# Performance work log

Hardware: AMD Instinct MI355X
Metric: run time of the kernel (lower is better)

## Reference

```python
import jax, jax.numpy as jnp
import numpy as np

H = 16        # heads
DH = 64       # dim_head
DM = 1024     # query_dim = context_dim
INNER = H * DH


def setup_inputs() -> dict:
    key = jax.random.key(0)
    ks = jax.random.split(key, 5)
    s = 0.02
    queries = jax.random.normal(ks[0], (2, 2048, DM), dtype=jnp.float32)
    Wq = jax.random.normal(ks[1], (DM, INNER), dtype=jnp.float32) * s
    Wkv = jax.random.normal(ks[2], (DM, 2 * INNER), dtype=jnp.float32) * s
    Wo = jax.random.normal(ks[3], (INNER, DM), dtype=jnp.float32) * s
    bo = jax.random.normal(ks[4], (DM,), dtype=jnp.float32) * s
    return {"queries": queries, "Wq": Wq, "Wkv": Wkv, "Wo": Wo, "bo": bo}


def reference(queries, Wq, Wkv, Wo, bo):
    b, n, _ = queries.shape
    scale = DH ** -0.5
    q = queries @ Wq                       # [b, n, inner]
    kv = queries @ Wkv                     # self-attention: context = queries
    k, v = jnp.split(kv, 2, axis=-1)
    # b n (h d) -> b h n d
    split_heads = lambda t: t.reshape(b, n, H, DH).transpose(0, 2, 1, 3)
    q, k, v = map(split_heads, (q, k, v))
    sim = jnp.einsum('bhid,bhjd->bhij', q, k) * scale
    attn = jax.nn.softmax(sim, axis=-1)    # dropout is identity (p=0 / eval)
    out = jnp.einsum('bhij,bhjd->bhid', attn, v)
    out = out.transpose(0, 2, 1, 3).reshape(b, n, INNER)
    return out @ Wo + bo
```

## Files before the change

kernel.cpp:

```cpp
#include <hip/hip_runtime.h>
#include <math.h>
#include <stdint.h>

typedef _Float16 half8v __attribute__((ext_vector_type(8)));
typedef _Float16 half4v __attribute__((ext_vector_type(4)));
typedef _Float16 half2v __attribute__((ext_vector_type(2)));
typedef __fp16 fp16x2 __attribute__((ext_vector_type(2)));
typedef float floatx4 __attribute__((ext_vector_type(4)));

#define MFMA16(a, b, c) __builtin_amdgcn_mfma_f32_16x16x32_f16(a, b, c, 0, 0, 0)

#define QSCALE 0.18033688011112f

__device__ __forceinline__ void gld_lds16(const void* g, void* l) {
  __builtin_amdgcn_global_load_lds(
      (const __attribute__((address_space(1))) uint32_t*)(uintptr_t)g,
      (__attribute__((address_space(3))) uint32_t*)(uintptr_t)l, 16, 0, 0);
}

__device__ __forceinline__ half2v pk16(float a, float b) {
  fp16x2 t = __builtin_amdgcn_cvt_pkrtz(a, b);
  return __builtin_bit_cast(half2v, t);
}

__global__ __launch_bounds__(256) void convert_x(
    const float* __restrict__ X, _Float16* __restrict__ X16)
{
  size_t gid = (size_t)blockIdx.x * 256 + threadIdx.x;
  const float4* src = (const float4*)(X) + gid * 2;
  float4 a = src[0], b = src[1];
  half8v h;
  h[0]=(_Float16)a.x; h[1]=(_Float16)a.y; h[2]=(_Float16)a.z; h[3]=(_Float16)a.w;
  h[4]=(_Float16)b.x; h[5]=(_Float16)b.y; h[6]=(_Float16)b.z; h[7]=(_Float16)b.w;
  *((half8v*)X16 + gid) = h;
}

__global__ __launch_bounds__(256) void transpose_w(
    const float* __restrict__ Wq, const float* __restrict__ Wkv,
    const float* __restrict__ Wo,
    _Float16* __restrict__ WqkvT, _Float16* __restrict__ WoT)
{
  __shared__ alignas(16) _Float16 Tt[64 * 68];

  int b = blockIdx.x;
  const float* src; _Float16* dst; int N, tk, tn;
  if (b < 256)      { src = Wq;  dst = WqkvT;                 N = 1024; tk = b & 15;        tn = b >> 4; }
  else if (b < 768) { src = Wkv; dst = WqkvT + (size_t)1024 * 1024; N = 2048; tk = (b - 256) & 15; tn = (b - 256) >> 4; }
  else              { src = Wo;  dst = WoT;                   N = 1024; tk = (b - 768) & 15; tn = (b - 768) >> 4; }

  const int t = threadIdx.x;
  {
    int kg = t >> 4, ng = t & 15;
    const float* sp = src + (size_t)(tk * 64 + kg * 4) * N + tn * 64 + ng * 4;
    float4 r0 = *(const float4*)(sp);
    float4 r1 = *(const float4*)(sp + N);
    float4 r2 = *(const float4*)(sp + 2 * N);
    float4 r3 = *(const float4*)(sp + 3 * N);
    half4v h;
    h[0]=(_Float16)r0.x; h[1]=(_Float16)r1.x; h[2]=(_Float16)r2.x; h[3]=(_Float16)r3.x;
    *(half4v*)&Tt[(ng * 4 + 0) * 68 + kg * 4] = h;
    h[0]=(_Float16)r0.y; h[1]=(_Float16)r1.y; h[2]=(_Float16)r2.y; h[3]=(_Float16)r3.y;
    *(half4v*)&Tt[(ng * 4 + 1) * 68 + kg * 4] = h;
    h[0]=(_Float16)r0.z; h[1]=(_Float16)r1.z; h[2]=(_Float16)r2.z; h[3]=(_Float16)r3.z;
    *(half4v*)&Tt[(ng * 4 + 2) * 68 + kg * 4] = h;
    h[0]=(_Float16)r0.w; h[1]=(_Float16)r1.w; h[2]=(_Float16)r2.w; h[3]=(_Float16)r3.w;
    *(half4v*)&Tt[(ng * 4 + 3) * 68 + kg * 4] = h;
  }
  __syncthreads();
  #pragma unroll
  for (int i = 0; i < 2; i++) {
    int idx = t + i * 256;
    int nl = idx >> 3, k8 = (idx & 7) * 8;
    half8v v = *(half8v*)&Tt[nl * 68 + k8];
    *(half8v*)(dst + (size_t)(tn * 64 + nl) * 1024 + tk * 64 + k8) = v;
  }
}

__global__ __launch_bounds__(256) void qkv_gemm(
    const _Float16* __restrict__ X16, const _Float16* __restrict__ WqkvT,
    _Float16* __restrict__ q_ws, _Float16* __restrict__ k_ws,
    _Float16* __restrict__ vT_ws)
{
  constexpr int K = 1024;
  __shared__ alignas(16) _Float16 As[128 * 32];
  __shared__ alignas(16) _Float16 Bs[128 * 32];

  const int m0 = blockIdx.x * 128;
  const int n0 = blockIdx.y * 128;

  const int tid  = threadIdx.x;
  const int wave = tid >> 6, lane = tid & 63;
  const int qd = lane >> 4, l15 = lane & 15;
  const int wr = (wave >> 1) * 64, wc = (wave & 1) * 64;
  const int r0i = tid >> 2, c0 = (tid & 3) * 8;

  floatx4 acc[4][4] = {};

  for (int k0 = 0; k0 < K; k0 += 32) {
    gld_lds16(X16 + (size_t)(m0 + r0i) * K + k0 + c0, &As[tid * 8]);
    gld_lds16(X16 + (size_t)(m0 + 64 + r0i) * K + k0 + c0, &As[(tid + 256) * 8]);
    gld_lds16(WqkvT + (size_t)(n0 + r0i) * K + k0 + c0, &Bs[tid * 8]);
    gld_lds16(WqkvT + (size_t)(n0 + 64 + r0i) * K + k0 + c0, &Bs[(tid + 256) * 8]);
    __syncthreads();
    half8v a[4], b[4];
    #pragma unroll
    for (int it = 0; it < 4; it++)
      a[it] = *(half8v*)&As[(wr + it * 16 + l15) * 32 + qd * 8];
    #pragma unroll
    for (int jt = 0; jt < 4; jt++)
      b[jt] = *(half8v*)&Bs[(wc + jt * 16 + l15) * 32 + qd * 8];
    #pragma unroll
    for (int it = 0; it < 4; it++)
      #pragma unroll
      for (int jt = 0; jt < 4; jt++)
        acc[it][jt] = MFMA16(a[it], b[jt], acc[it][jt]);
    __syncthreads();
  }

  #pragma unroll
  for (int it = 0; it < 4; it++) {
    #pragma unroll
    for (int jt = 0; jt < 4; jt++) {
      #pragma unroll
      for (int r = 0; r < 4; r++) {
        int m = m0 + wr + it * 16 + qd * 4 + r;
        int n = n0 + wc + jt * 16 + l15;
        float val = acc[it][jt][r];
        int bb = m >> 11, nn = m & 2047;
        if (n0 < 1024) {
          int h = n >> 6, d = n & 63;
          q_ws[(((size_t)bb * 16 + h) * 2048 + nn) * 64 + d] = (_Float16)(val * QSCALE);
        } else if (n0 < 2048) {
          int c = n - 1024, h = c >> 6, d = c & 63;
          k_ws[(((size_t)bb * 16 + h) * 2048 + nn) * 64 + d] = (_Float16)val;
        } else {
          int c = n - 2048, h = c >> 6, d = c & 63;
          vT_ws[(((size_t)bb * 16 + h) * 64 + d) * 2048 + nn] = (_Float16)val;
        }
      }
    }
  }
}

__device__ __forceinline__ int swz(int row, int blk) {
  return row * 64 + ((blk ^ (row & 7)) << 3);
}

__global__ __launch_bounds__(128, 2) void attn_kernel(
    const _Float16* __restrict__ q_ws, const _Float16* __restrict__ k_ws,
    const _Float16* __restrict__ vT_ws, _Float16* __restrict__ aout)
{
  constexpr int N = 2048;
  __shared__ alignas(16) _Float16 Qs[64 * 64];
  __shared__ alignas(16) _Float16 Ks[2][64 * 64];
  __shared__ alignas(16) _Float16 Vts[2][64 * 64];

  const int id = blockIdx.x;
  const int bh = ((id >> 8) << 3) | (id & 7);
  const int qt = (id >> 3) & 31;

  const _Float16* Qp = q_ws + (size_t)bh * N * 64;
  const _Float16* Kp = k_ws + (size_t)bh * N * 64;
  const _Float16* Vp = vT_ws + (size_t)bh * 64 * N;

  const int tid = threadIdx.x, wave = tid >> 6, lane = tid & 63;
  const int qd = lane >> 4, l15 = lane & 15;
  const int q0 = qt * 64;
  const int wbase = wave * 32;

  #pragma unroll
  for (int i = 0; i < 4; i++) {
    int idx = tid + i * 128;
    int r = idx >> 3, blk = idx & 7;
    *(half8v*)&Qs[swz(r, blk)] =
        *(const half8v*)(Qp + (size_t)(q0 + r) * 64 + blk * 8);
  }
  __syncthreads();
  half8v qf[2][2];
  #pragma unroll
  for (int m = 0; m < 2; m++)
    #pragma unroll
    for (int ks = 0; ks < 2; ks++)
      qf[m][ks] = *(half8v*)&Qs[swz(wbase + m * 16 + l15, ks * 4 + qd)];

  floatx4 o[2][4] = {};
  float lsum[2] = {};

  half8v kpre[4], vpre[4];
  #pragma unroll
  for (int i = 0; i < 4; i++) {
    int idx = tid + i * 128;
    int r = idx >> 3, c8 = (idx & 7) * 8;
    kpre[i] = *(const half8v*)(Kp + (size_t)r * 64 + c8);
    vpre[i] = *(const half8v*)(Vp + (size_t)r * N + c8);
  }
  #pragma unroll
  for (int i = 0; i < 4; i++) {
    int idx = tid + i * 128;
    int r = idx >> 3, blk = idx & 7;
    *(half8v*)&Ks[0][swz(r, blk)]  = kpre[i];
    *(half8v*)&Vts[0][swz(r, blk)] = vpre[i];
  }

  int p = 0;
  for (int kv0 = 0; kv0 < N; kv0 += 64) {
    const bool more = (kv0 + 64) < N;
    if (more) {
      int kvn = kv0 + 64;
      #pragma unroll
      for (int i = 0; i < 4; i++) {
        int idx = tid + i * 128;
        int r = idx >> 3, c8 = (idx & 7) * 8;
        kpre[i] = *(const half8v*)(Kp + (size_t)(kvn + r) * 64 + c8);
        vpre[i] = *(const half8v*)(Vp + (size_t)r * N + kvn + c8);
      }
    }
    __syncthreads();

    floatx4 s[4][2] = {};
    #pragma unroll
    for (int ks = 0; ks < 2; ks++) {
      half8v kf[4];
      #pragma unroll
      for (int nt = 0; nt < 4; nt++)
        kf[nt] = *(half8v*)&Ks[p][swz(nt * 16 + l15, ks * 4 + qd)];
      #pragma unroll
      for (int nt = 0; nt < 4; nt++)
        #pragma unroll
        for (int m = 0; m < 2; m++)
          s[nt][m] = MFMA16(kf[nt], qf[m][ks], s[nt][m]);
    }

    #pragma unroll
    for (int m = 0; m < 2; m++) {
      #pragma unroll
      for (int nt = 0; nt < 4; nt++) {
        float p0 = __builtin_amdgcn_exp2f(s[nt][m][0]);
        float p1 = __builtin_amdgcn_exp2f(s[nt][m][1]);
        float p2 = __builtin_amdgcn_exp2f(s[nt][m][2]);
        float p3 = __builtin_amdgcn_exp2f(s[nt][m][3]);
        lsum[m] += (p0 + p1) + (p2 + p3);
        half2v h01 = pk16(p0, p1);
        half2v h23 = pk16(p2, p3);
        half4v pk;
        pk[0] = h01[0]; pk[1] = h01[1]; pk[2] = h23[0]; pk[3] = h23[1];
        *(half4v*)&Qs[swz(wbase + m * 16 + l15, 2 * nt + (qd >> 1)) +
                      (qd & 1) * 4] = pk;
      }
    }

    #pragma unroll
    for (int ks = 0; ks < 2; ks++) {
      half8v pf[2], vf[4];
      #pragma unroll
      for (int m = 0; m < 2; m++)
        pf[m] = *(half8v*)&Qs[swz(wbase + m * 16 + l15, 4 * ks + qd)];
      #pragma unroll
      for (int nt = 0; nt < 4; nt++)
        vf[nt] = *(half8v*)&Vts[p][swz(nt * 16 + l15, 4 * ks + qd)];
      #pragma unroll
      for (int m = 0; m < 2; m++)
        #pragma unroll
        for (int nt = 0; nt < 4; nt++)
          o[m][nt] = MFMA16(pf[m], vf[nt], o[m][nt]);
    }

    if (more) {
      #pragma unroll
      for (int i = 0; i < 4; i++) {
        int idx = tid + i * 128;
        int r = idx >> 3, blk = idx & 7;
        *(half8v*)&Ks[p ^ 1][swz(r, blk)]  = kpre[i];
        *(half8v*)&Vts[p ^ 1][swz(r, blk)] = vpre[i];
      }
    }
    p ^= 1;
  }

  #pragma unroll
  for (int m = 0; m < 2; m++) {
    lsum[m] += __shfl_xor(lsum[m], 16);
    lsum[m] += __shfl_xor(lsum[m], 32);
  }

  const int bb = bh >> 4, hh = bh & 15;
  #pragma unroll
  for (int m = 0; m < 2; m++) {
    #pragma unroll
    for (int r = 0; r < 4; r++) {
      float inv = 1.0f / __shfl(lsum[m], qd * 4 + r);
      int n = q0 + wbase + m * 16 + qd * 4 + r;
      #pragma unroll
      for (int dt = 0; dt < 4; dt++) {
        int d = dt * 16 + l15;
        aout[((size_t)(bb * 2048 + n)) * 1024 + hh * 64 + d] =
            (_Float16)(o[m][dt][r] * inv);
      }
    }
  }
}

__global__ __launch_bounds__(256) void out_gemm(
    const _Float16* __restrict__ A, const _Float16* __restrict__ WoT,
    const float* __restrict__ bo, float* __restrict__ Out)
{
  constexpr int K = 1024;
  __shared__ alignas(16) _Float16 As[128 * 32];
  __shared__ alignas(16) _Float16 Bs[128 * 32];

  const int m0 = blockIdx.x * 128;
  const int n0 = blockIdx.y * 128;
  const int tid = threadIdx.x;
  const int wave = tid >> 6, lane = tid & 63;
  const int qd = lane >> 4, l15 = lane & 15;
  const int wr = (wave >> 1) * 64, wc = (wave & 1) * 64;
  const int r0i = tid >> 2, c0 = (tid & 3) * 8;

  floatx4 acc[4][4] = {};

  for (int k0 = 0; k0 < K; k0 += 32) {
    gld_lds16(A + (size_t)(m0 + r0i) * K + k0 + c0, &As[tid * 8]);
    gld_lds16(A + (size_t)(m0 + 64 + r0i) * K + k0 + c0, &As[(tid + 256) * 8]);
    gld_lds16(WoT + (size_t)(n0 + r0i) * K + k0 + c0, &Bs[tid * 8]);
    gld_lds16(WoT + (size_t)(n0 + 64 + r0i) * K + k0 + c0, &Bs[(tid + 256) * 8]);
    __syncthreads();
    half8v a[4], b[4];
    #pragma unroll
    for (int it = 0; it < 4; it++)
      a[it] = *(half8v*)&As[(wr + it * 16 + l15) * 32 + qd * 8];
    #pragma unroll
    for (int jt = 0; jt < 4; jt++)
      b[jt] = *(half8v*)&Bs[(wc + jt * 16 + l15) * 32 + qd * 8];
    #pragma unroll
    for (int it = 0; it < 4; it++)
      #pragma unroll
      for (int jt = 0; jt < 4; jt++)
        acc[it][jt] = MFMA16(a[it], b[jt], acc[it][jt]);
    __syncthreads();
  }

  #pragma unroll
  for (int it = 0; it < 4; it++) {
    #pragma unroll
    for (int jt = 0; jt < 4; jt++) {
      int n = n0 + wc + jt * 16 + l15;
      float bias = bo[n];
      #pragma unroll
      for (int r = 0; r < 4; r++) {
        int m = m0 + wr + it * 16 + qd * 4 + r;
        Out[(size_t)m * 1024 + n] = acc[it][jt][r] + bias;
      }
    }
  }
}

extern "C" void kernel_launch(void* const* d_in, const int* in_sizes, int n_in,
                              void* d_out, int out_size, void* d_ws, size_t ws_size,
                              hipStream_t stream) {
  const float* X   = (const float*)d_in[0];
  const float* Wq  = (const float*)d_in[1];
  const float* Wkv = (const float*)d_in[2];
  const float* Wo  = (const float*)d_in[3];
  const float* bo  = (const float*)d_in[4];
  float* out = (float*)d_out;

  const size_t M4 = (size_t)4 * 1024 * 1024;
  _Float16* q_ws   = (_Float16*)d_ws;
  _Float16* k_ws   = q_ws + M4;
  _Float16* vT_ws  = k_ws + M4;
  _Float16* X16    = vT_ws + M4;
  _Float16* WqkvT  = X16 + M4;
  _Float16* WoT    = WqkvT + (size_t)3 * 1024 * 1024;
  _Float16* aout   = X16;

  convert_x<<<2048, 256, 0, stream>>>(X, X16);
  transpose_w<<<1024, 256, 0, stream>>>(Wq, Wkv, Wo, WqkvT, WoT);
  qkv_gemm<<<dim3(32, 24), 256, 0, stream>>>(X16, WqkvT, q_ws, k_ws, vT_ws);
  attn_kernel<<<1024, 128, 0, stream>>>(q_ws, k_ws, vT_ws, aout);
  out_gemm<<<dim3(32, 8), 256, 0, stream>>>(aout, WoT, bo, out);
}
```

Measured before the change: 197.8 us.

## Enlarge attention query tile to 128 rows per block and restructure QK loop

Each attention block now processes 128 query rows instead of 64, with each wave owning 64 rows, which halves the grid and halves the K/V tile traffic per query row. The QK^T computation is reorganised to loop over key subtiles, computing and exponentiating one 16-column strip at a time, which limits live score registers. The trade-off is higher accumulator register pressure (16 output tiles per wave), which may lower occupancy, and only 512 blocks to spread across the CUs.

```diff
diff --git a/kernel.cpp b/kernel.cpp
--- a/kernel.cpp
+++ b/kernel.cpp
@@ -151,13 +151,13 @@
     const _Float16* __restrict__ vT_ws, _Float16* __restrict__ aout)
 {
   constexpr int N = 2048;
-  __shared__ alignas(16) _Float16 Qs[64 * 64];
+  __shared__ alignas(16) _Float16 Qs[128 * 64];
   __shared__ alignas(16) _Float16 Ks[2][64 * 64];
   __shared__ alignas(16) _Float16 Vts[2][64 * 64];
 
   const int id = blockIdx.x;
-  const int bh = ((id >> 8) << 3) | (id & 7);
-  const int qt = (id >> 3) & 31;
+  const int bh = ((id >> 7) << 3) | (id & 7);
+  const int qt = (id >> 3) & 15;
 
   const _Float16* Qp = q_ws + (size_t)bh * N * 64;
   const _Float16* Kp = k_ws + (size_t)bh * N * 64;
@@ -165,26 +165,26 @@
 
   const int tid = threadIdx.x, wave = tid >> 6, lane = tid & 63;
   const int qd = lane >> 4, l15 = lane & 15;
-  const int q0 = qt * 64;
-  const int wbase = wave * 32;
-
-  #pragma unroll
-  for (int i = 0; i < 4; i++) {
+  const int q0 = qt * 128;
+  const int wbase = wave * 64;
+
+  #pragma unroll
+  for (int i = 0; i < 8; i++) {
     int idx = tid + i * 128;
     int r = idx >> 3, blk = idx & 7;
     *(half8v*)&Qs[swz(r, blk)] =
         *(const half8v*)(Qp + (size_t)(q0 + r) * 64 + blk * 8);
   }
   __syncthreads();
-  half8v qf[2][2];
-  #pragma unroll
-  for (int m = 0; m < 2; m++)
+  half8v qf[4][2];
+  #pragma unroll
+  for (int m = 0; m < 4; m++)
     #pragma unroll
     for (int ks = 0; ks < 2; ks++)
       qf[m][ks] = *(half8v*)&Qs[swz(wbase + m * 16 + l15, ks * 4 + qd)];
 
-  floatx4 o[2][4] = {};
-  float lsum[2] = {};
+  floatx4 o[4][4] = {};
+  float lsum[4] = {};
 
   half8v kpre[4], vpre[4];
   #pragma unroll
@@ -217,28 +217,22 @@
     }
     __syncthreads();
 
-    floatx4 s[4][2] = {};
-    #pragma unroll
-    for (int ks = 0; ks < 2; ks++) {
-      half8v kf[4];
-      #pragma unroll
-      for (int nt = 0; nt < 4; nt++)
-        kf[nt] = *(half8v*)&Ks[p][swz(nt * 16 + l15, ks * 4 + qd)];
-      #pragma unroll
-      for (int nt = 0; nt < 4; nt++)
-        #pragma unroll
-        for (int m = 0; m < 2; m++)
-          s[nt][m] = MFMA16(kf[nt], qf[m][ks], s[nt][m]);
-    }
-
-    #pragma unroll
-    for (int m = 0; m < 2; m++) {
-      #pragma unroll
-      for (int nt = 0; nt < 4; nt++) {
-        float p0 = __builtin_amdgcn_exp2f(s[nt][m][0]);
-        float p1 = __builtin_amdgcn_exp2f(s[nt][m][1]);
-        float p2 = __builtin_amdgcn_exp2f(s[nt][m][2]);
-        float p3 = __builtin_amdgcn_exp2f(s[nt][m][3]);
+    #pragma unroll
+    for (int nt = 0; nt < 4; nt++) {
+      half8v kf0 = *(half8v*)&Ks[p][swz(nt * 16 + l15, qd)];
+      half8v kf1 = *(half8v*)&Ks[p][swz(nt * 16 + l15, 4 + qd)];
+      floatx4 s[4];
+      #pragma unroll
+      for (int m = 0; m < 4; m++) {
+        s[m] = MFMA16(kf0, qf[m][0], floatx4{});
+        s[m] = MFMA16(kf1, qf[m][1], s[m]);
+      }
+      #pragma unroll
+      for (int m = 0; m < 4; m++) {
+        float p0 = __builtin_amdgcn_exp2f(s[m][0]);
+        float p1 = __builtin_amdgcn_exp2f(s[m][1]);
+        float p2 = __builtin_amdgcn_exp2f(s[m][2]);
+        float p3 = __builtin_amdgcn_exp2f(s[m][3]);
         lsum[m] += (p0 + p1) + (p2 + p3);
         half2v h01 = pk16(p0, p1);
         half2v h23 = pk16(p2, p3);
@@ -251,18 +245,18 @@
 
     #pragma unroll
     for (int ks = 0; ks < 2; ks++) {
-      half8v pf[2], vf[4];
-      #pragma unroll
-      for (int m = 0; m < 2; m++)
+      half8v pf[4], vf[4];
+      #pragma unroll
+      for (int m = 0; m < 4; m++)
         pf[m] = *(half8v*)&Qs[swz(wbase + m * 16 + l15, 4 * ks + qd)];
       #pragma unroll
-      for (int nt = 0; nt < 4; nt++)
-        vf[nt] = *(half8v*)&Vts[p][swz(nt * 16 + l15, 4 * ks + qd)];
-      #pragma unroll
-      for (int m = 0; m < 2; m++)
+      for (int dt = 0; dt < 4; dt++)
+        vf[dt] = *(half8v*)&Vts[p][swz(dt * 16 + l15, 4 * ks + qd)];
+      #pragma unroll
+      for (int m = 0; m < 4; m++)
         #pragma unroll
-        for (int nt = 0; nt < 4; nt++)
-          o[m][nt] = MFMA16(pf[m], vf[nt], o[m][nt]);
+        for (int dt = 0; dt < 4; dt++)
+          o[m][dt] = MFMA16(pf[m], vf[dt], o[m][dt]);
     }
 
     if (more) {
@@ -278,14 +272,14 @@
   }
 
   #pragma unroll
-  for (int m = 0; m < 2; m++) {
+  for (int m = 0; m < 4; m++) {
     lsum[m] += __shfl_xor(lsum[m], 16);
     lsum[m] += __shfl_xor(lsum[m], 32);
   }
 
   const int bb = bh >> 4, hh = bh & 15;
   #pragma unroll
-  for (int m = 0; m < 2; m++) {
+  for (int m = 0; m < 4; m++) {
     #pragma unroll
     for (int r = 0; r < 4; r++) {
       float inv = 1.0f / __shfl(lsum[m], qd * 4 + r);
@@ -376,6 +370,6 @@
   convert_x<<<2048, 256, 0, stream>>>(X, X16);
   transpose_w<<<1024, 256, 0, stream>>>(Wq, Wkv, Wo, WqkvT, WoT);
   qkv_gemm<<<dim3(32, 24), 256, 0, stream>>>(X16, WqkvT, q_ws, k_ws, vT_ws);
-  attn_kernel<<<1024, 128, 0, stream>>>(q_ws, k_ws, vT_ws, aout);
+  attn_kernel<<<512, 128, 0, stream>>>(q_ws, k_ws, vT_ws, aout);
   out_gemm<<<dim3(32, 8), 256, 0, stream>>>(aout, WoT, bo, out);
 }
```

After: 208.5 us. 1.05x slower.
